# Optimization experiments

Measured on AMD Instinct MI355X. Metric: run time of the kernel, lower is better.

## Reference

```python
import jax, jax.numpy as jnp
import numpy as np

N_NODES = 100000
IN_DIM = 256
HID = 128      # per-branch output_dim; concat -> 2*HID
N_CLASSES = 7
B, S0, S1 = 512, 25, 10
EPS = 1e-12


def setup_inputs() -> dict:
    key = jax.random.key(0)
    ks = jax.random.split(key, 16)
    d = {
        "ids": jax.random.randint(ks[0], (B,), 0, N_NODES),
        "ids1": jax.random.randint(ks[1], (B * S0,), 0, N_NODES),
        "ids2": jax.random.randint(ks[2], (B * S0 * S1,), 0, N_NODES),
        "feats": jax.random.normal(ks[3], (N_NODES, IN_DIM), dtype=jnp.float32),
        # layer-1 aggregator (input 256 -> concat 256)
        "W_x1": jax.random.normal(ks[4], (IN_DIM, HID), dtype=jnp.float32) * 0.05,
        "b_x1": jnp.zeros((HID,), dtype=jnp.float32),
        "W_n1": jax.random.normal(ks[5], (IN_DIM, HID), dtype=jnp.float32) * 0.05,
        "b_n1": jnp.zeros((HID,), dtype=jnp.float32),
        # layer-2 aggregator (input 256 -> concat 256)
        "W_x2": jax.random.normal(ks[6], (2 * HID, HID), dtype=jnp.float32) * 0.05,
        "b_x2": jnp.zeros((HID,), dtype=jnp.float32),
        "W_n2": jax.random.normal(ks[7], (2 * HID, HID), dtype=jnp.float32) * 0.05,
        "b_n2": jnp.zeros((HID,), dtype=jnp.float32),
        # final classifier
        "W_fc": jax.random.normal(ks[8], (2 * HID, N_CLASSES), dtype=jnp.float32) * 0.05,
        "b_fc": jnp.zeros((N_CLASSES,), dtype=jnp.float32),
    }
    return d


def _agg(x, neibs, Wx, bx, Wn, bn, act):
    # neibs: [len(x)*k, d] -> mean over k sampled neighbors per node
    m = neibs.reshape(x.shape[0], -1, neibs.shape[-1]).mean(axis=1)
    out = jnp.concatenate([x @ Wx + bx, m @ Wn + bn], axis=1)
    return act(out)


def reference(ids, ids1, ids2, feats,
              W_x1, b_x1, W_n1, b_n1,
              W_x2, b_x2, W_n2, b_n2,
              W_fc, b_fc):
    # multi-hop feature gathers (IdentityPrep)
    f0 = feats[ids]    # [B, d]
    f1 = feats[ids1]   # [B*S0, d]
    f2 = feats[ids2]   # [B*S0*S1, d]
    # aggregator layer 1 (relu), applied across consecutive hops
    h0 = _agg(f0, f1, W_x1, b_x1, W_n1, b_n1, jax.nn.relu)  # [B, 2*HID]
    h1 = _agg(f1, f2, W_x1, b_x1, W_n1, b_n1, jax.nn.relu)  # [B*S0, 2*HID]
    # aggregator layer 2 (no activation)
    g0 = _agg(h0, h1, W_x2, b_x2, W_n2, b_n2, lambda v: v)  # [B, 2*HID]
    # F.normalize(dim=1)
    out = g0 / jnp.maximum(jnp.linalg.norm(g0, axis=1, keepdims=True), EPS)
    return out @ W_fc + b_fc
```

## Files before the change

### kernel.cpp

```cpp
#include <hip/hip_runtime.h>
#include <hip/hip_bf16.h>


typedef __bf16 bf16x8 __attribute__((ext_vector_type(8)));
typedef __bf16 bf16x4 __attribute__((ext_vector_type(4)));
typedef float  f32x4  __attribute__((ext_vector_type(4)));

constexpr int IN    = 256;
constexpr int HIDC  = 128;
constexpr int ROWS1 = 512 * 25;

__global__ __launch_bounds__(256) void k_wprep(
    const float* __restrict__ Wx, const float* __restrict__ Wn,
    __bf16* __restrict__ WtH, __bf16* __restrict__ WtL)
{
    const int j = blockIdx.x;
    const int k = threadIdx.x;
    const float v = (j < HIDC) ? Wx[(size_t)k * HIDC + j]
                               : Wn[(size_t)k * HIDC + (j - HIDC)];
    const __bf16 h = (__bf16)v;
    const __bf16 l = (__bf16)(v - (float)h);
    const size_t o = (size_t)j * IN + k;
    WtH[o] = h;
    WtL[o] = l;
}

__global__ __launch_bounds__(512) void k_fused(
    const int* __restrict__ ids1, const int* __restrict__ ids2,
    const float* __restrict__ feats,
    const __bf16* __restrict__ WtH, const __bf16* __restrict__ WtL,
    const float* __restrict__ bx, const float* __restrict__ bn,
    __bf16* __restrict__ h1)
{
    __shared__ __bf16 a0[16 * IN];
    __shared__ __bf16 a1[16 * IN];
    const int tid  = threadIdx.x;
    const int w    = tid >> 6;
    const int lane = tid & 63;
    const int r0   = blockIdx.x * 16;

    {
        const int rA = r0 + 2 * w;
        const int rB = rA + 1;
        float4 vx0, vx1, vn0[10], vn1[10];
        vx0 = ((const float4*)(feats + (size_t)ids1[rA] * IN))[lane];
        vx1 = ((const float4*)(feats + (size_t)ids1[rB] * IN))[lane];
        #pragma unroll
        for (int kk = 0; kk < 10; ++kk)
            vn0[kk] = ((const float4*)(feats + (size_t)ids2[rA * 10 + kk] * IN))[lane];
        #pragma unroll
        for (int kk = 0; kk < 10; ++kk)
            vn1[kk] = ((const float4*)(feats + (size_t)ids2[rB * 10 + kk] * IN))[lane];

        float4 s0 = make_float4(0.f, 0.f, 0.f, 0.f);
        float4 s1 = make_float4(0.f, 0.f, 0.f, 0.f);
        #pragma unroll
        for (int kk = 0; kk < 10; ++kk) {
            s0.x += vn0[kk].x; s0.y += vn0[kk].y; s0.z += vn0[kk].z; s0.w += vn0[kk].w;
            s1.x += vn1[kk].x; s1.y += vn1[kk].y; s1.z += vn1[kk].z; s1.w += vn1[kk].w;
        }

        const int rrA = 2 * w,  rrB = 2 * w + 1;
        const int eA = (rrA << 8) + lane * 4;
        const int eB = (rrB << 8) + lane * 4;
        const int eAs = eA ^ ((rrA & 7) << 3);
        const int eBs = eB ^ ((rrB & 7) << 3);
        const bf16x4 x0v = {(__bf16)vx0.x, (__bf16)vx0.y, (__bf16)vx0.z, (__bf16)vx0.w};
        const bf16x4 x1v = {(__bf16)vx1.x, (__bf16)vx1.y, (__bf16)vx1.z, (__bf16)vx1.w};
        const bf16x4 m0v = {(__bf16)(s0.x * 0.1f), (__bf16)(s0.y * 0.1f),
                            (__bf16)(s0.z * 0.1f), (__bf16)(s0.w * 0.1f)};
        const bf16x4 m1v = {(__bf16)(s1.x * 0.1f), (__bf16)(s1.y * 0.1f),
                            (__bf16)(s1.z * 0.1f), (__bf16)(s1.w * 0.1f)};
        *(bf16x4*)&a0[eAs] = x0v;
        *(bf16x4*)&a0[eBs] = x1v;
        *(bf16x4*)&a1[eAs] = m0v;
        *(bf16x4*)&a1[eBs] = m1v;
    }
    __syncthreads();

    const int br  = w & 1;
    const int cg  = w >> 1;
    const int l15 = lane & 15;
    const int lk  = lane >> 4;
    const __bf16* __restrict__ As = br ? a1 : a0;
    const __bf16* __restrict__ WH = WtH + (size_t)br * HIDC * IN;
    const __bf16* __restrict__ WL = WtL + (size_t)br * HIDC * IN;

    const f32x4 z = {0.f, 0.f, 0.f, 0.f};
    f32x4 acc[2] = {z, z};

    for (int k0 = 0; k0 < IN; k0 += 32) {
        int ea = (l15 << 8) + k0 + lk * 8;
        ea ^= (l15 & 7) << 3;
        const bf16x8 a = *(const bf16x8*)&As[ea];
        #pragma unroll
        for (int ct = 0; ct < 2; ++ct) {
            const size_t eb = (size_t)(cg * 32 + ct * 16 + l15) * IN + k0 + lk * 8;
            const bf16x8 bH = *(const bf16x8*)&WH[eb];
            const bf16x8 bL = *(const bf16x8*)&WL[eb];
            acc[ct] = __builtin_amdgcn_mfma_f32_16x16x32_bf16(a, bH, acc[ct], 0, 0, 0);
            acc[ct] = __builtin_amdgcn_mfma_f32_16x16x32_bf16(a, bL, acc[ct], 0, 0, 0);
        }
    }

    const float* __restrict__ bias = br ? bn : bx;
    #pragma unroll
    for (int ct = 0; ct < 2; ++ct) {
        const int colL = cg * 32 + ct * 16 + l15;
        const float bv = bias[colL];
        #pragma unroll
        for (int q = 0; q < 4; ++q) {
            const int rr = lk * 4 + q;
            h1[(size_t)(r0 + rr) * IN + br * HIDC + colL] =
                (__bf16)fmaxf(acc[ct][q] + bv, 0.f);
        }
    }
}

__global__ __launch_bounds__(512) void k_out(
    const int* __restrict__ ids, const int* __restrict__ ids1,
    const float* __restrict__ feats, const __bf16* __restrict__ h1,
    const float* __restrict__ Wx1, const float* __restrict__ bx1,
    const float* __restrict__ Wn1, const float* __restrict__ bn1,
    const float* __restrict__ Wx2, const float* __restrict__ bx2,
    const float* __restrict__ Wn2, const float* __restrict__ bn2,
    const float* __restrict__ Wfc, const float* __restrict__ bfc,
    float* __restrict__ out)
{
    __shared__ float x0[IN];
    __shared__ float m1[IN];
    __shared__ float mh[IN];
    __shared__ float h0[IN];
    __shared__ float g0[IN];
    __shared__ float partA[2][IN];
    __shared__ float partB[2][IN];
    __shared__ float red[8];
    __shared__ float fcred[7][4];
    const int i   = blockIdx.x;
    const int tid = threadIdx.x;
    const int c   = tid & 255;
    const int h   = tid >> 8;

    {
        float v1[13], v2[13];
        #pragma unroll
        for (int t = 0; t < 13; ++t) {
            const int kk = h * 13 + t;
            const int kc = kk < 25 ? kk : 24;
            const int r  = i * 25 + kc;
            v1[t] = feats[(size_t)ids1[r] * IN + c];
            v2[t] = (float)h1[(size_t)r * IN + c];
        }
        float s = 0.f, sh = 0.f;
        #pragma unroll
        for (int t = 0; t < 13; ++t) {
            const float msk = (h * 13 + t < 25) ? 1.f : 0.f;
            s  += msk * v1[t];
            sh += msk * v2[t];
        }
        if (h == 0) x0[c] = feats[(size_t)ids[i] * IN + c];
        partA[h][c] = s;
        partB[h][c] = sh;
    }
    __syncthreads();
    if (h == 0) m1[c] = (partA[0][c] + partA[1][c]) * 0.04f;
    else        mh[c] = (partB[0][c] + partB[1][c]) * 0.04f;
    __syncthreads();

    const int  jj = c & 127;
    const bool nb = (c >= 128);
    {
        const float* __restrict__ W = nb ? Wn1 : Wx1;
        const float* __restrict__ X = nb ? m1 : x0;
        float acc = 0.f;
        #pragma unroll 8
        for (int k = h * 128; k < h * 128 + 128; ++k)
            acc = fmaf(X[k], W[(size_t)k * HIDC + jj], acc);
        partA[h][c] = acc;
    }
    __syncthreads();
    if (h == 0)
        h0[c] = fmaxf(partA[0][c] + partA[1][c] + (nb ? bn1 : bx1)[jj], 0.f);
    __syncthreads();
    {
        const float* __restrict__ W = nb ? Wn2 : Wx2;
        const float* __restrict__ X = nb ? mh : h0;
        float acc = 0.f;
        #pragma unroll 8
        for (int k = h * 128; k < h * 128 + 128; ++k)
            acc = fmaf(X[k], W[(size_t)k * HIDC + jj], acc);
        partB[h][c] = acc;
    }
    __syncthreads();
    if (h == 0)
        g0[c] = partB[0][c] + partB[1][c] + (nb ? bn2 : bx2)[jj];
    __syncthreads();

    {
        const float gv = g0[c];
        float sq = gv * gv;
        #pragma unroll
        for (int off = 32; off > 0; off >>= 1) sq += __shfl_down(sq, off);
        if ((tid & 63) == 0) red[tid >> 6] = sq;
    }
    __syncthreads();
    const float total = (red[0] + red[1] + red[2] + red[3] +
                         red[4] + red[5] + red[6] + red[7]) * 0.5f;
    const float inv = 1.f / fmaxf(sqrtf(total), 1e-12f);
    const float p = g0[c] * inv;

    const int qbase = h * 4;
    const int qn    = h ? 3 : 4;
    for (int q = qbase; q < qbase + qn; ++q) {
        float t = p * Wfc[(size_t)c * 7 + q];
        #pragma unroll
        for (int off = 32; off > 0; off >>= 1) t += __shfl_down(t, off);
        if ((tid & 63) == 0) fcred[q][(tid >> 6) & 3] = t;
    }
    __syncthreads();
    if (tid < 7) {
        out[(size_t)i * 7 + tid] =
            fcred[tid][0] + fcred[tid][1] + fcred[tid][2] + fcred[tid][3] + bfc[tid];
    }
}

extern "C" void kernel_launch(void* const* d_in, const int* in_sizes, int n_in,
                              void* d_out, int out_size, void* d_ws, size_t ws_size,
                              hipStream_t stream) {
    const int*   ids   = (const int*)d_in[0];
    const int*   ids1  = (const int*)d_in[1];
    const int*   ids2  = (const int*)d_in[2];
    const float* feats = (const float*)d_in[3];
    const float* Wx1   = (const float*)d_in[4];
    const float* bx1   = (const float*)d_in[5];
    const float* Wn1   = (const float*)d_in[6];
    const float* bn1   = (const float*)d_in[7];
    const float* Wx2   = (const float*)d_in[8];
    const float* bx2   = (const float*)d_in[9];
    const float* Wn2   = (const float*)d_in[10];
    const float* bn2   = (const float*)d_in[11];
    const float* Wfc   = (const float*)d_in[12];
    const float* bfc   = (const float*)d_in[13];
    float* out = (float*)d_out;

    __bf16* h1  = (__bf16*)d_ws;
    __bf16* WtH = h1 + (size_t)ROWS1 * IN;
    __bf16* WtL = WtH + (size_t)IN * IN;

    k_wprep<<<256, 256, 0, stream>>>(Wx1, Wn1, WtH, WtL);
    k_fused<<<ROWS1 / 16, 512, 0, stream>>>(ids1, ids2, feats, WtH, WtL,
                                            bx1, bn1, h1);
    k_out<<<512, 512, 0, stream>>>(ids, ids1, feats, h1,
                                   Wx1, bx1, Wn1, bn1,
                                   Wx2, bx2, Wn2, bn2,
                                   Wfc, bfc, out);
}
```

Measured before the change: 71.48 us.

## Split fused gather+GEMM into separate gather and register-resident-weight GEMM kernels

The fused kernel is split into a pure gather kernel that writes bf16 self and neighbour-mean rows to workspace, and a GEMM kernel in which each wave keeps its weight column slice in registers and loops over a 128-row strip. The final kernel reads the bf16 gathered self features instead of re-gathering fp32 rows from feats. This aims to decouple the latency-bound random gather from the MFMA work and stop re-reading weights for every 16-row tile, at the cost of an extra launch and a global round trip for the intermediate activations. k_out's neighbour mean for the first layer now comes from bf16-rounded features.

```diff
diff --git a/kernel.cpp b/kernel.cpp
--- a/kernel.cpp
+++ b/kernel.cpp
@@ -25,101 +25,82 @@
     WtL[o] = l;
 }
 
-__global__ __launch_bounds__(512) void k_fused(
+__global__ __launch_bounds__(512) void k_gath(
     const int* __restrict__ ids1, const int* __restrict__ ids2,
     const float* __restrict__ feats,
+    __bf16* __restrict__ A0, __bf16* __restrict__ A1)
+{
+    const int r    = blockIdx.x * 8 + (threadIdx.x >> 6);
+    const int lane = threadIdx.x & 63;
+    const int base = r * 10;
+
+    const float4 vx = ((const float4*)(feats + (size_t)ids1[r] * IN))[lane];
+    float4 s = make_float4(0.f, 0.f, 0.f, 0.f);
+    #pragma unroll
+    for (int kk = 0; kk < 10; ++kk) {
+        const float4 v = ((const float4*)(feats + (size_t)ids2[base + kk] * IN))[lane];
+        s.x += v.x; s.y += v.y; s.z += v.z; s.w += v.w;
+    }
+    const bf16x4 a0 = {(__bf16)vx.x, (__bf16)vx.y, (__bf16)vx.z, (__bf16)vx.w};
+    const bf16x4 a1 = {(__bf16)(s.x * 0.1f), (__bf16)(s.y * 0.1f),
+                       (__bf16)(s.z * 0.1f), (__bf16)(s.w * 0.1f)};
+    *(bf16x4*)&A0[(size_t)r * IN + lane * 4] = a0;
+    *(bf16x4*)&A1[(size_t)r * IN + lane * 4] = a1;
+}
+
+__global__ __launch_bounds__(256) void k_gemm(
+    const __bf16* __restrict__ A0, const __bf16* __restrict__ A1,
     const __bf16* __restrict__ WtH, const __bf16* __restrict__ WtL,
     const float* __restrict__ bx, const float* __restrict__ bn,
     __bf16* __restrict__ h1)
 {
-    __shared__ __bf16 a0[16 * IN];
-    __shared__ __bf16 a1[16 * IN];
     const int tid  = threadIdx.x;
-    const int w    = tid >> 6;
     const int lane = tid & 63;
-    const int r0   = blockIdx.x * 16;
-
-    {
-        const int rA = r0 + 2 * w;
-        const int rB = rA + 1;
-        float4 vx0, vx1, vn0[10], vn1[10];
-        vx0 = ((const float4*)(feats + (size_t)ids1[rA] * IN))[lane];
-        vx1 = ((const float4*)(feats + (size_t)ids1[rB] * IN))[lane];
-        #pragma unroll
-        for (int kk = 0; kk < 10; ++kk)
-            vn0[kk] = ((const float4*)(feats + (size_t)ids2[rA * 10 + kk] * IN))[lane];
-        #pragma unroll
-        for (int kk = 0; kk < 10; ++kk)
-            vn1[kk] = ((const float4*)(feats + (size_t)ids2[rB * 10 + kk] * IN))[lane];
-
-        float4 s0 = make_float4(0.f, 0.f, 0.f, 0.f);
-        float4 s1 = make_float4(0.f, 0.f, 0.f, 0.f);
-        #pragma unroll
-        for (int kk = 0; kk < 10; ++kk) {
-            s0.x += vn0[kk].x; s0.y += vn0[kk].y; s0.z += vn0[kk].z; s0.w += vn0[kk].w;
-            s1.x += vn1[kk].x; s1.y += vn1[kk].y; s1.z += vn1[kk].z; s1.w += vn1[kk].w;
-        }
-
-        const int rrA = 2 * w,  rrB = 2 * w + 1;
-        const int eA = (rrA << 8) + lane * 4;
-        const int eB = (rrB << 8) + lane * 4;
-        const int eAs = eA ^ ((rrA & 7) << 3);
-        const int eBs = eB ^ ((rrB & 7) << 3);
-        const bf16x4 x0v = {(__bf16)vx0.x, (__bf16)vx0.y, (__bf16)vx0.z, (__bf16)vx0.w};
-        const bf16x4 x1v = {(__bf16)vx1.x, (__bf16)vx1.y, (__bf16)vx1.z, (__bf16)vx1.w};
-        const bf16x4 m0v = {(__bf16)(s0.x * 0.1f), (__bf16)(s0.y * 0.1f),
-                            (__bf16)(s0.z * 0.1f), (__bf16)(s0.w * 0.1f)};
-        const bf16x4 m1v = {(__bf16)(s1.x * 0.1f), (__bf16)(s1.y * 0.1f),
-                            (__bf16)(s1.z * 0.1f), (__bf16)(s1.w * 0.1f)};
-        *(bf16x4*)&a0[eAs] = x0v;
-        *(bf16x4*)&a0[eBs] = x1v;
-        *(bf16x4*)&a1[eAs] = m0v;
-        *(bf16x4*)&a1[eBs] = m1v;
-    }
-    __syncthreads();
-
-    const int br  = w & 1;
-    const int cg  = w >> 1;
-    const int l15 = lane & 15;
-    const int lk  = lane >> 4;
-    const __bf16* __restrict__ As = br ? a1 : a0;
-    const __bf16* __restrict__ WH = WtH + (size_t)br * HIDC * IN;
-    const __bf16* __restrict__ WL = WtL + (size_t)br * HIDC * IN;
-
-    const f32x4 z = {0.f, 0.f, 0.f, 0.f};
-    f32x4 acc[2] = {z, z};
-
-    for (int k0 = 0; k0 < IN; k0 += 32) {
-        int ea = (l15 << 8) + k0 + lk * 8;
-        ea ^= (l15 & 7) << 3;
-        const bf16x8 a = *(const bf16x8*)&As[ea];
-        #pragma unroll
-        for (int ct = 0; ct < 2; ++ct) {
-            const size_t eb = (size_t)(cg * 32 + ct * 16 + l15) * IN + k0 + lk * 8;
-            const bf16x8 bH = *(const bf16x8*)&WH[eb];
-            const bf16x8 bL = *(const bf16x8*)&WL[eb];
-            acc[ct] = __builtin_amdgcn_mfma_f32_16x16x32_bf16(a, bH, acc[ct], 0, 0, 0);
-            acc[ct] = __builtin_amdgcn_mfma_f32_16x16x32_bf16(a, bL, acc[ct], 0, 0, 0);
-        }
-    }
-
-    const float* __restrict__ bias = br ? bn : bx;
+    const int l15  = lane & 15;
+    const int lk   = lane >> 4;
+    const int gw   = blockIdx.x * 4 + (tid >> 6);
+    const int br   = gw & 1;
+    const int cg   = (gw >> 1) & 7;
+    const int strip = gw >> 4;
+
+    const __bf16* __restrict__ Ap = br ? A1 : A0;
+    const int colG = br * HIDC + cg * 16 + l15;
+    const float bv = (br ? bn : bx)[cg * 16 + l15];
+
+    bf16x8 bh[8], bl[8];
     #pragma unroll
-    for (int ct = 0; ct < 2; ++ct) {
-        const int colL = cg * 32 + ct * 16 + l15;
-        const float bv = bias[colL];
+    for (int kb = 0; kb < 8; ++kb) {
+        const size_t eb = (size_t)colG * IN + kb * 32 + lk * 8;
+        bh[kb] = *(const bf16x8*)&WtH[eb];
+        bl[kb] = *(const bf16x8*)&WtL[eb];
+    }
+
+    #pragma unroll 2
+    for (int t = 0; t < 8; ++t) {
+        const int r0 = strip * 128 + t * 16;
+        bf16x8 a[8];
+        #pragma unroll
+        for (int kb = 0; kb < 8; ++kb)
+            a[kb] = *(const bf16x8*)&Ap[(size_t)(r0 + l15) * IN + kb * 32 + lk * 8];
+
+        f32x4 acc = {0.f, 0.f, 0.f, 0.f};
+        #pragma unroll
+        for (int kb = 0; kb < 8; ++kb) {
+            acc = __builtin_amdgcn_mfma_f32_16x16x32_bf16(a[kb], bh[kb], acc, 0, 0, 0);
+            acc = __builtin_amdgcn_mfma_f32_16x16x32_bf16(a[kb], bl[kb], acc, 0, 0, 0);
+        }
         #pragma unroll
         for (int q = 0; q < 4; ++q) {
-            const int rr = lk * 4 + q;
-            h1[(size_t)(r0 + rr) * IN + br * HIDC + colL] =
-                (__bf16)fmaxf(acc[ct][q] + bv, 0.f);
+            h1[(size_t)(r0 + lk * 4 + q) * IN + colG] =
+                (__bf16)fmaxf(acc[q] + bv, 0.f);
         }
     }
 }
 
 __global__ __launch_bounds__(512) void k_out(
     const int* __restrict__ ids, const int* __restrict__ ids1,
-    const float* __restrict__ feats, const __bf16* __restrict__ h1,
+    const float* __restrict__ feats,
+    const __bf16* __restrict__ A0, const __bf16* __restrict__ h1,
     const float* __restrict__ Wx1, const float* __restrict__ bx1,
     const float* __restrict__ Wn1, const float* __restrict__ bn1,
     const float* __restrict__ Wx2, const float* __restrict__ bx2,
@@ -148,7 +129,7 @@
             const int kk = h * 13 + t;
             const int kc = kk < 25 ? kk : 24;
             const int r  = i * 25 + kc;
-            v1[t] = feats[(size_t)ids1[r] * IN + c];
+            v1[t] = (float)A0[(size_t)r * IN + c];
             v2[t] = (float)h1[(size_t)r * IN + c];
         }
         float s = 0.f, sh = 0.f;
@@ -243,14 +224,16 @@
     const float* bfc   = (const float*)d_in[13];
     float* out = (float*)d_out;
 
-    __bf16* h1  = (__bf16*)d_ws;
-    __bf16* WtH = h1 + (size_t)ROWS1 * IN;
+    __bf16* A0  = (__bf16*)d_ws;
+    __bf16* A1  = A0  + (size_t)ROWS1 * IN;
+    __bf16* h1  = A1  + (size_t)ROWS1 * IN;
+    __bf16* WtH = h1  + (size_t)ROWS1 * IN;
     __bf16* WtL = WtH + (size_t)IN * IN;
 
     k_wprep<<<256, 256, 0, stream>>>(Wx1, Wn1, WtH, WtL);
-    k_fused<<<ROWS1 / 16, 512, 0, stream>>>(ids1, ids2, feats, WtH, WtL,
-                                            bx1, bn1, h1);
-    k_out<<<512, 512, 0, stream>>>(ids, ids1, feats, h1,
+    k_gath<<<ROWS1 / 8, 512, 0, stream>>>(ids1, ids2, feats, A0, A1);
+    k_gemm<<<400, 256, 0, stream>>>(A0, A1, WtH, WtL, bx1, bn1, h1);
+    k_out<<<512, 512, 0, stream>>>(ids, ids1, feats, A0, h1,
                                    Wx1, bx1, Wn1, bn1,
                                    Wx2, bx2, Wn2, bn2,
                                    Wfc, bfc, out);
```

New measurement: 69.68 us. 2.5% less time.
